# Kernel tuning notes

Measured on AMD Instinct MI355X. Metric: run time of the kernel, lower is better.

## Reference

```python
import jax, jax.numpy as jnp
import numpy as np
from jax.ops import segment_sum

N_NODES = 100000
N_EDGES = 1600000
N_GRAPHS = 128
HIDDEN = 128
N_CLASSES = 10


def setup_inputs() -> dict:
    key = jax.random.key(0)
    ks = jax.random.split(key, 8)
    src = jax.random.randint(ks[0], (N_EDGES,), 0, N_NODES, dtype=jnp.int32)
    dst = jax.random.randint(ks[1], (N_EDGES,), 0, N_NODES, dtype=jnp.int32)
    graph_ids = jnp.sort(jax.random.randint(ks[2], (N_NODES,), 0, N_GRAPHS, dtype=jnp.int32))
    W1 = jax.random.normal(ks[3], (1, HIDDEN), dtype=jnp.float32)
    b1 = jnp.zeros((HIDDEN,), jnp.float32)
    W2 = jax.random.normal(ks[4], (HIDDEN, HIDDEN), dtype=jnp.float32) * 0.05
    b2 = jnp.zeros((HIDDEN,), jnp.float32)
    Wc = jax.random.normal(ks[5], (HIDDEN, N_CLASSES), dtype=jnp.float32) * 0.05
    bc = jnp.zeros((N_CLASSES,), jnp.float32)
    return {"src": src, "dst": dst, "graph_ids": graph_ids,
            "W1": W1, "b1": b1, "W2": W2, "b2": b2, "Wc": Wc, "bc": bc}


def _graph_conv(h, src, dst, norm_src, norm_dst, W, b, n_nodes):
    # DGL GraphConv, norm='both': D_out^{-1/2} gather -> scatter-sum -> W -> D_in^{-1/2} -> +b
    hs = h * norm_src[:, None]
    agg = segment_sum(hs[src], dst, num_segments=n_nodes)  # [N, F_in]
    return agg @ W * norm_dst[:, None] + b


def reference(src, dst, graph_ids, W1, b1, W2, b2, Wc, bc):
    n_nodes = graph_ids.shape[0]
    ones_e = jnp.ones(src.shape[0], jnp.float32)
    indeg = segment_sum(ones_e, dst, num_segments=n_nodes)
    outdeg = segment_sum(ones_e, src, num_segments=n_nodes)
    norm_src = jnp.clip(outdeg, 1.0, None) ** -0.5
    norm_dst = jnp.clip(indeg, 1.0, None) ** -0.5

    h = indeg[:, None]  # node feature = in-degree, [N, 1]
    h = jax.nn.relu(_graph_conv(h, src, dst, norm_src, norm_dst, W1, b1, n_nodes))
    h = jax.nn.relu(_graph_conv(h, src, dst, norm_src, norm_dst, W2, b2, n_nodes))

    # dgl.mean_nodes: per-graph mean pooling
    sums = segment_sum(h, graph_ids, num_segments=N_GRAPHS)          # [G, H]
    cnts = segment_sum(jnp.ones(n_nodes, jnp.float32), graph_ids, num_segments=N_GRAPHS)
    hg = sums / jnp.clip(cnts, 1.0, None)[:, None]
    return hg @ Wc + bc  # [G, n_classes]
```

## Files before the change

kernel.cpp:

```cpp
#include <hip/hip_runtime.h>

#define N_NODES   100000
#define N_EDGES   1600000
#define N_GRAPHS  128
#define HIDDEN    128
#define N_CLASSES 10

#define BSH   9
#define BSZ   512
#define NBUCK 196
#define CAP   16384
#define PCH   4096

typedef unsigned int   uint;
typedef unsigned short ushort;
typedef unsigned char  uchar;
typedef unsigned long long ull;

__global__ __launch_bounds__(256)
void k_part(const int* __restrict__ src, const int* __restrict__ dst,
            unsigned* __restrict__ bcur1, unsigned* __restrict__ bcur2,
            unsigned* __restrict__ tmp1, ushort* __restrict__ tmp2, int nE) {
    __shared__ unsigned histD[256], histS[256], scanT[256];
    __shared__ unsigned lcurD[256], lcurS[256], baseD[256], baseS[256];
    __shared__ unsigned stag1[PCH];
    __shared__ ushort   stag2[PCH];
    __shared__ uchar    stagB1[PCH], stagB2[PCH];
    int t = threadIdx.x;
    int e0 = blockIdx.x * PCH;
    int e1 = min(e0 + PCH, nE);
    histD[t] = 0; histS[t] = 0;
    __syncthreads();
    for (int e = e0 + t; e < e1; e += 256) {
        atomicAdd(&histD[dst[e] >> BSH], 1u);
        atomicAdd(&histS[src[e] >> BSH], 1u);
    }
    __syncthreads();
    unsigned vD = histD[t];
    scanT[t] = vD; __syncthreads();
    for (int off = 1; off < 256; off <<= 1) {
        unsigned add = (t >= off) ? scanT[t - off] : 0u;
        __syncthreads();
        scanT[t] += add;
        __syncthreads();
    }
    unsigned exD = scanT[t] - vD;
    if (vD > 0) { unsigned g = atomicAdd(&bcur1[t], vD); baseD[t] = (unsigned)t * CAP + g - exD; }
    lcurD[t] = exD;
    __syncthreads();
    unsigned vS = histS[t];
    scanT[t] = vS; __syncthreads();
    for (int off = 1; off < 256; off <<= 1) {
        unsigned add = (t >= off) ? scanT[t - off] : 0u;
        __syncthreads();
        scanT[t] += add;
        __syncthreads();
    }
    unsigned exS = scanT[t] - vS;
    if (vS > 0) { unsigned g = atomicAdd(&bcur2[t], vS); baseS[t] = (unsigned)t * CAP + g - exS; }
    lcurS[t] = exS;
    __syncthreads();
    for (int e = e0 + t; e < e1; e += 256) {
        int d = dst[e], s = src[e];
        int bd = d >> BSH, bs = s >> BSH;
        unsigned p1 = atomicAdd(&lcurD[bd], 1u);
        stag1[p1]  = ((unsigned)(d & (BSZ - 1)) << 17) | (unsigned)s;
        stagB1[p1] = (uchar)bd;
        unsigned p2 = atomicAdd(&lcurS[bs], 1u);
        stag2[p2]  = (ushort)(s & (BSZ - 1));
        stagB2[p2] = (uchar)bs;
    }
    __syncthreads();
    int cntE = e1 - e0;
    for (int i = t; i < cntE; i += 256) {
        unsigned b = stagB1[i];
        unsigned a = baseD[b] + (unsigned)i;
        if (a < (b + 1u) * CAP) tmp1[a] = stag1[i];
    }
    for (int i = t; i < cntE; i += 256) {
        unsigned b = stagB2[i];
        unsigned a = baseS[b] + (unsigned)i;
        if (a < (b + 1u) * CAP) tmp2[a] = stag2[i];
    }
}

__global__ __launch_bounds__(1024)
void k_ind_hs0(const unsigned* __restrict__ bcur1, const unsigned* __restrict__ tmp1,
               const unsigned* __restrict__ bcur2, const ushort* __restrict__ tmp2,
               unsigned* __restrict__ indeg, float* __restrict__ ns,
               float* __restrict__ hs0) {
    __shared__ unsigned cin[BSZ], cout[BSZ];
    int b = blockIdx.x, t = threadIdx.x;
    if (t < BSZ) { cin[t] = 0; cout[t] = 0; }
    __syncthreads();
    unsigned f1 = min(bcur1[b], (unsigned)CAP);
    const unsigned* tp1 = tmp1 + (size_t)b * CAP;
    for (unsigned i = t; i < f1; i += 1024) atomicAdd(&cin[tp1[i] >> 17], 1u);
    unsigned f2 = min(bcur2[b], (unsigned)CAP);
    const ushort* tp2 = tmp2 + (size_t)b * CAP;
    for (unsigned i = t; i < f2; i += 1024) atomicAdd(&cout[tp2[i]], 1u);
    __syncthreads();
    if (t < BSZ) {
        int n = b * BSZ + t;
        if (n < N_NODES) {
            unsigned ci = cin[t], co = cout[t];
            float nsv = rsqrtf(fmaxf((float)co, 1.0f));
            indeg[n] = ci;
            ns[n]    = nsv;
            hs0[n]   = (float)ci * nsv;
        }
    }
}

__global__ void k_segtable(const float* __restrict__ W1, const float* __restrict__ b1,
                           const float* __restrict__ W2,
                           float* __restrict__ U, float* __restrict__ V,
                           float* __restrict__ ts) {
    __shared__ float s[128];
    int t = threadIdx.x;
    {
        float w = W1[t], bb = b1[t];
        s[t] = (w != 0.0f) ? (-bb / w) : 1e30f;
    }
    __syncthreads();
    for (int k = 2; k <= 128; k <<= 1) {
        for (int j = k >> 1; j > 0; j >>= 1) {
            int ixj = t ^ j;
            if (ixj > t) {
                float a = s[t], bb = s[ixj];
                bool up = ((t & k) == 0);
                if (up ? (a > bb) : (a < bb)) { s[t] = bb; s[ixj] = a; }
            }
            __syncthreads();
        }
    }
    if (blockIdx.x == 0) ts[t] = s[t];
    int sg = blockIdx.x;
    float a_rep;
    if (sg == 0)        a_rep = s[0]   - 1.0f;
    else if (sg == 128) a_rep = s[127] + 1.0f;
    else                a_rep = 0.5f * (s[sg - 1] + s[sg]);
    float u = 0.0f, v = 0.0f;
    for (int j = 0; j < 128; ++j) {
        float w = W1[j], bb = b1[j];
        if (a_rep * w + bb > 0.0f) {
            float w2 = W2[j * HIDDEN + t];
            u += w * w2;
            v += bb * w2;
        }
    }
    U[sg * HIDDEN + t] = u;
    V[sg * HIDDEN + t] = v;
}

__global__ __launch_bounds__(1024)
void k_conv1_info(const unsigned* __restrict__ bcur1, const unsigned* __restrict__ tmp1,
                  const float* __restrict__ hs0, const unsigned* __restrict__ indeg,
                  const float* __restrict__ ns, const float* __restrict__ ts,
                  float4* __restrict__ info) {
    __shared__ float acc[BSZ];
    __shared__ float sts[128];
    int b = blockIdx.x, t = threadIdx.x;
    if (t < BSZ) acc[t] = 0.0f;
    if (t < 128) sts[t] = ts[t];
    __syncthreads();
    unsigned f1 = min(bcur1[b], (unsigned)CAP);
    const unsigned* tp = tmp1 + (size_t)b * CAP;
    for (unsigned i = t; i < f1; i += 1024) {
        unsigned e = tp[i];
        atomicAdd(&acc[e >> 17], hs0[e & 0x1FFFFu]);
    }
    __syncthreads();
    if (t < BSZ) {
        int n = b * BSZ + t;
        if (n < N_NODES) {
            float nd = rsqrtf(fmaxf((float)indeg[n], 1.0f));
            float a  = acc[t] * nd;
            float nsv = ns[n];
            int sg = 0;
            #pragma unroll
            for (int j = 0; j < 128; ++j) sg += (sts[j] < a) ? 1 : 0;
            info[n] = make_float4(nsv * a, nsv, __int_as_float(sg), nd);
        }
    }
}

__global__ __launch_bounds__(1024)
void k_conv2_pool(const unsigned* __restrict__ bcur1, const unsigned* __restrict__ tmp1,
                  const float4* __restrict__ info, const unsigned* __restrict__ indeg,
                  const float* __restrict__ U, const float* __restrict__ V,
                  const int* __restrict__ graph_ids, const float* __restrict__ b2,
                  float* __restrict__ pool, float* __restrict__ cnt) {
    __shared__ float sc[BSZ], sn2[BSZ];
    __shared__ ull   ssq[BSZ];
    __shared__ float sND[BSZ];
    __shared__ int   sGr[BSZ];
    int b = blockIdx.x, t = threadIdx.x;
    if (t < BSZ) { sc[t] = 0.0f; sn2[t] = 0.0f; ssq[t] = 0ull; }
    __syncthreads();
    unsigned f1 = min(bcur1[b], (unsigned)CAP);
    const unsigned* tp = tmp1 + (size_t)b * CAP;
    for (unsigned i = t; i < f1; i += 1024) {
        unsigned e = tp[i];
        unsigned dl = e >> 17, s = e & 0x1FFFFu;
        float4 nf = info[s];
        unsigned sg = (unsigned)__float_as_int(nf.z);
        atomicAdd(&sc[dl],  nf.x);
        atomicAdd(&sn2[dl], nf.y);
        atomicAdd(&ssq[dl], ((ull)(sg * sg) << 32) | (ull)sg);
    }
    if (t < BSZ) {
        int n = b * BSZ + t;
        if (n < N_NODES) { sND[t] = info[n].w; sGr[t] = graph_ids[n]; }
    }
    __syncthreads();

    int w = t >> 6, lane = t & 63;
    int base = b * BSZ;
    float bb0 = b2[lane], bb1 = b2[64 + lane];
    int gcur = -1;
    float racc0 = 0.0f, racc1 = 0.0f, cl = 0.0f;

    for (int i = w * 32; i < w * 32 + 32; ++i) {
        int n = base + i;
        if (n >= N_NODES) break;
        unsigned cntN = indeg[n];
        ull pk = ssq[i];
        unsigned S1 = (unsigned)pk, S2 = (unsigned)(pk >> 32);
        float acc0, acc1;
        if ((ull)cntN * S2 == (ull)S1 * S1) {
            unsigned sg = cntN ? (S1 / cntN) : 0u;
            float A = sc[i], B = sn2[i];
            const float* Ur = U + sg * HIDDEN;
            const float* Vr = V + sg * HIDDEN;
            acc0 = A * Ur[lane]      + B * Vr[lane];
            acc1 = A * Ur[64 + lane] + B * Vr[64 + lane];
        } else {
            acc0 = 0.0f; acc1 = 0.0f;
            for (unsigned j = 0; j < f1; ++j) {
                unsigned e = tp[j];
                if ((int)(e >> 17) == i) {
                    float4 nf = info[e & 0x1FFFFu];
                    unsigned sg = (unsigned)__float_as_int(nf.z);
                    const float* Ur = U + sg * HIDDEN;
                    const float* Vr = V + sg * HIDDEN;
                    acc0 += nf.x * Ur[lane]      + nf.y * Vr[lane];
                    acc1 += nf.x * Ur[64 + lane] + nf.y * Vr[64 + lane];
                }
            }
        }
        float nd = sND[i];
        float r0 = fmaxf(nd * acc0 + bb0, 0.0f);
        float r1 = fmaxf(nd * acc1 + bb1, 0.0f);
        int g = sGr[i];
        if (g != gcur) {
            if (gcur >= 0) {
                atomicAdd(&pool[gcur * HIDDEN + lane],      racc0);
                atomicAdd(&pool[gcur * HIDDEN + 64 + lane], racc1);
                if (lane == 0) atomicAdd(&cnt[gcur], cl);
            }
            gcur = g; racc0 = 0.0f; racc1 = 0.0f; cl = 0.0f;
        }
        racc0 += r0; racc1 += r1; cl += 1.0f;
    }
    if (gcur >= 0) {
        atomicAdd(&pool[gcur * HIDDEN + lane],      racc0);
        atomicAdd(&pool[gcur * HIDDEN + 64 + lane], racc1);
        if (lane == 0) atomicAdd(&cnt[gcur], cl);
    }
}

__global__ void k_final(const float* __restrict__ pool, const float* __restrict__ cnt,
                        const float* __restrict__ Wc, const float* __restrict__ bc,
                        float* __restrict__ out) {
    int t = blockIdx.x * blockDim.x + threadIdx.x;
    if (t >= N_GRAPHS * N_CLASSES) return;
    int g = t / N_CLASSES, c = t % N_CLASSES;
    float inv = 1.0f / fmaxf(cnt[g], 1.0f);
    float acc = bc[c];
    for (int j = 0; j < HIDDEN; ++j)
        acc += pool[g * HIDDEN + j] * inv * Wc[j * N_CLASSES + c];
    out[t] = acc;
}

extern "C" void kernel_launch(void* const* d_in, const int* in_sizes, int n_in,
                              void* d_out, int out_size, void* d_ws, size_t ws_size,
                              hipStream_t stream) {
    const int*   src       = (const int*)d_in[0];
    const int*   dst       = (const int*)d_in[1];
    const int*   graph_ids = (const int*)d_in[2];
    const float* W1        = (const float*)d_in[3];
    const float* b1        = (const float*)d_in[4];
    const float* W2        = (const float*)d_in[5];
    const float* b2        = (const float*)d_in[6];
    const float* Wc        = (const float*)d_in[7];
    const float* bc        = (const float*)d_in[8];
    float* out = (float*)d_out;

    char* ws = (char*)d_ws;
    size_t off = 0;
    auto alloc = [&](size_t elems) { void* p = ws + off; off += elems * 4; return p; };

    unsigned* bcur1 = (unsigned*)alloc(256);
    unsigned* bcur2 = (unsigned*)alloc(256);
    float*    pool  = (float*)   alloc(N_GRAPHS * HIDDEN);
    float*    cnt   = (float*)   alloc(N_GRAPHS);
    size_t zero_bytes = off;
    float4*   info  = (float4*)  alloc((size_t)N_NODES * 4);
    unsigned* tmp1  = (unsigned*)alloc((size_t)NBUCK * CAP);
    ushort*   tmp2  = (ushort*)  alloc((size_t)NBUCK * CAP / 2);
    unsigned* indeg = (unsigned*)alloc(N_NODES);
    float*    nsA   = (float*)   alloc(N_NODES);
    float*    hs0   = (float*)   alloc(N_NODES);
    float*    ts    = (float*)   alloc(128);
    float*    U     = (float*)   alloc(129 * HIDDEN);
    float*    V     = (float*)   alloc(129 * HIDDEN);

    hipMemsetAsync(d_ws, 0, zero_bytes, stream);

    int pblocks = (N_EDGES + PCH - 1) / PCH;
    k_part      <<<pblocks, 256, 0, stream>>>(src, dst, bcur1, bcur2, tmp1, tmp2, N_EDGES);
    k_ind_hs0   <<<NBUCK, 1024, 0, stream>>>(bcur1, tmp1, bcur2, tmp2, indeg, nsA, hs0);
    k_segtable  <<<129, 128, 0, stream>>>(W1, b1, W2, U, V, ts);
    k_conv1_info<<<NBUCK, 1024, 0, stream>>>(bcur1, tmp1, hs0, indeg, nsA, ts, info);
    k_conv2_pool<<<NBUCK, 1024, 0, stream>>>(bcur1, tmp1, info, indeg, U, V, graph_ids, b2, pool, cnt);
    k_final     <<<(N_GRAPHS * N_CLASSES + 255) / 256, 256, 0, stream>>>(pool, cnt, Wc, bc, out);
}
```

Before: 201.3 us.

## Build per-bucket CSR and switch conv kernels to per-node gather

The in-degree kernel now prefix-scans per-node in-degrees within each bucket and scatters source ids into a CSR layout. Both conv kernels then run one thread per node, summing over that node's CSR row instead of doing shared-memory atomics over the bucket's edge list. Conv2 replaces the sum/sum-of-squares uniformity test with a min/max segment check. This also lets the fallback path walk only the node's own edges rather than rescanning the whole bucket. The cost is an extra CSR write pass plus per-thread loops whose length varies with degree.

After: 191.2 us. 5.0% less time.

```diff
diff --git a/kernel.cpp b/kernel.cpp
--- a/kernel.cpp
+++ b/kernel.cpp
@@ -15,7 +15,6 @@
 typedef unsigned int   uint;
 typedef unsigned short ushort;
 typedef unsigned char  uchar;
-typedef unsigned long long ull;
 
 __global__ __launch_bounds__(256)
 void k_part(const int* __restrict__ src, const int* __restrict__ dst,
@@ -85,11 +84,12 @@
 }
 
 __global__ __launch_bounds__(1024)
-void k_ind_hs0(const unsigned* __restrict__ bcur1, const unsigned* __restrict__ tmp1,
+void k_ind_csr(const unsigned* __restrict__ bcur1, const unsigned* __restrict__ tmp1,
                const unsigned* __restrict__ bcur2, const ushort* __restrict__ tmp2,
                unsigned* __restrict__ indeg, float* __restrict__ ns,
-               float* __restrict__ hs0) {
-    __shared__ unsigned cin[BSZ], cout[BSZ];
+               float* __restrict__ hs0, int* __restrict__ rs,
+               int* __restrict__ csr) {
+    __shared__ unsigned cin[BSZ], cout[BSZ], pref[BSZ], lcur[BSZ];
     int b = blockIdx.x, t = threadIdx.x;
     if (t < BSZ) { cin[t] = 0; cout[t] = 0; }
     __syncthreads();
@@ -100,7 +100,18 @@
     const ushort* tp2 = tmp2 + (size_t)b * CAP;
     for (unsigned i = t; i < f2; i += 1024) atomicAdd(&cout[tp2[i]], 1u);
     __syncthreads();
+    unsigned v = (t < BSZ) ? cin[t] : 0u;
+    if (t < BSZ) pref[t] = v;
+    __syncthreads();
+    for (int off = 1; off < BSZ; off <<= 1) {
+        unsigned add = (t < BSZ && t >= off) ? pref[t - off] : 0u;
+        __syncthreads();
+        if (t < BSZ) pref[t] += add;
+        __syncthreads();
+    }
     if (t < BSZ) {
+        unsigned excl = pref[t] - v;
+        lcur[t] = excl;
         int n = b * BSZ + t;
         if (n < N_NODES) {
             unsigned ci = cin[t], co = cout[t];
@@ -108,7 +119,15 @@
             indeg[n] = ci;
             ns[n]    = nsv;
             hs0[n]   = (float)ci * nsv;
-        }
+            rs[n]    = (int)(b * CAP + excl);
+        }
+    }
+    __syncthreads();
+    int* cb = csr + (size_t)b * CAP;
+    for (unsigned i = t; i < f1; i += 1024) {
+        unsigned e = tp1[i];
+        unsigned pos = atomicAdd(&lcur[e >> 17], 1u);
+        cb[pos] = (int)(e & 0x1FFFFu);
     }
 }
 
@@ -153,105 +172,96 @@
     V[sg * HIDDEN + t] = v;
 }
 
-__global__ __launch_bounds__(1024)
-void k_conv1_info(const unsigned* __restrict__ bcur1, const unsigned* __restrict__ tmp1,
+__global__ __launch_bounds__(256)
+void k_conv1_info(const int* __restrict__ rs, const int* __restrict__ csr,
                   const float* __restrict__ hs0, const unsigned* __restrict__ indeg,
                   const float* __restrict__ ns, const float* __restrict__ ts,
-                  float4* __restrict__ info) {
-    __shared__ float acc[BSZ];
+                  float4* __restrict__ info, int nN) {
     __shared__ float sts[128];
-    int b = blockIdx.x, t = threadIdx.x;
-    if (t < BSZ) acc[t] = 0.0f;
-    if (t < 128) sts[t] = ts[t];
-    __syncthreads();
-    unsigned f1 = min(bcur1[b], (unsigned)CAP);
-    const unsigned* tp = tmp1 + (size_t)b * CAP;
-    for (unsigned i = t; i < f1; i += 1024) {
-        unsigned e = tp[i];
-        atomicAdd(&acc[e >> 17], hs0[e & 0x1FFFFu]);
-    }
-    __syncthreads();
-    if (t < BSZ) {
-        int n = b * BSZ + t;
-        if (n < N_NODES) {
-            float nd = rsqrtf(fmaxf((float)indeg[n], 1.0f));
-            float a  = acc[t] * nd;
-            float nsv = ns[n];
-            int sg = 0;
-            #pragma unroll
-            for (int j = 0; j < 128; ++j) sg += (sts[j] < a) ? 1 : 0;
-            info[n] = make_float4(nsv * a, nsv, __int_as_float(sg), nd);
-        }
-    }
-}
-
-__global__ __launch_bounds__(1024)
-void k_conv2_pool(const unsigned* __restrict__ bcur1, const unsigned* __restrict__ tmp1,
+    if (threadIdx.x < 128) sts[threadIdx.x] = ts[threadIdx.x];
+    __syncthreads();
+    int n = blockIdx.x * 256 + threadIdx.x;
+    if (n >= nN) return;
+    int r0 = rs[n];
+    int c  = (int)indeg[n];
+    float a = 0.0f;
+    #pragma unroll 4
+    for (int k = 0; k < c; ++k) a += hs0[csr[r0 + k]];
+    float nd = rsqrtf(fmaxf((float)c, 1.0f));
+    a *= nd;
+    float nsv = ns[n];
+    int sg = 0;
+    #pragma unroll
+    for (int j = 0; j < 128; ++j) sg += (sts[j] < a) ? 1 : 0;
+    info[n] = make_float4(nsv * a, nsv, __int_as_float(sg), nd);
+}
+
+__global__ __launch_bounds__(256)
+void k_conv2_pool(const int* __restrict__ rs, const int* __restrict__ csr,
                   const float4* __restrict__ info, const unsigned* __restrict__ indeg,
                   const float* __restrict__ U, const float* __restrict__ V,
                   const int* __restrict__ graph_ids, const float* __restrict__ b2,
-                  float* __restrict__ pool, float* __restrict__ cnt) {
-    __shared__ float sc[BSZ], sn2[BSZ];
-    __shared__ ull   ssq[BSZ];
-    __shared__ float sND[BSZ];
-    __shared__ int   sGr[BSZ];
-    int b = blockIdx.x, t = threadIdx.x;
-    if (t < BSZ) { sc[t] = 0.0f; sn2[t] = 0.0f; ssq[t] = 0ull; }
-    __syncthreads();
-    unsigned f1 = min(bcur1[b], (unsigned)CAP);
-    const unsigned* tp = tmp1 + (size_t)b * CAP;
-    for (unsigned i = t; i < f1; i += 1024) {
-        unsigned e = tp[i];
-        unsigned dl = e >> 17, s = e & 0x1FFFFu;
-        float4 nf = info[s];
-        unsigned sg = (unsigned)__float_as_int(nf.z);
-        atomicAdd(&sc[dl],  nf.x);
-        atomicAdd(&sn2[dl], nf.y);
-        atomicAdd(&ssq[dl], ((ull)(sg * sg) << 32) | (ull)sg);
-    }
-    if (t < BSZ) {
-        int n = b * BSZ + t;
-        if (n < N_NODES) { sND[t] = info[n].w; sGr[t] = graph_ids[n]; }
+                  float* __restrict__ pool, float* __restrict__ cnt, int nN) {
+    __shared__ float sA[256], sB[256], sND[256];
+    __shared__ int   sSg[256], sGr[256], sR[256], sC[256];
+    int blockBase = blockIdx.x * 256;
+    int t = threadIdx.x;
+    int n = blockBase + t;
+
+    if (n < nN) {
+        int r0 = rs[n], c = (int)indeg[n];
+        float A = 0.0f, B = 0.0f;
+        int mn = 255, mx = 0;
+        #pragma unroll 4
+        for (int k = 0; k < c; ++k) {
+            float4 nf = info[csr[r0 + k]];
+            int sg = __float_as_int(nf.z);
+            A += nf.x; B += nf.y;
+            mn = min(mn, sg); mx = max(mx, sg);
+        }
+        sA[t] = A; sB[t] = B;
+        sSg[t] = (mn << 8) | mx;
+        sR[t] = r0; sC[t] = c;
+        sND[t] = info[n].w;
+        sGr[t] = graph_ids[n];
     }
     __syncthreads();
 
     int w = t >> 6, lane = t & 63;
-    int base = b * BSZ;
+    int n0 = blockBase + 64 * w;
+    if (n0 >= nN) return;
+    int n1 = min(n0 + 64, nN);
+
     float bb0 = b2[lane], bb1 = b2[64 + lane];
     int gcur = -1;
     float racc0 = 0.0f, racc1 = 0.0f, cl = 0.0f;
 
-    for (int i = w * 32; i < w * 32 + 32; ++i) {
-        int n = base + i;
-        if (n >= N_NODES) break;
-        unsigned cntN = indeg[n];
-        ull pk = ssq[i];
-        unsigned S1 = (unsigned)pk, S2 = (unsigned)(pk >> 32);
+    for (int node = n0; node < n1; ++node) {
+        int i = node - blockBase;
+        int pk = sSg[i], mn = pk >> 8, mx = pk & 255;
         float acc0, acc1;
-        if ((ull)cntN * S2 == (ull)S1 * S1) {
-            unsigned sg = cntN ? (S1 / cntN) : 0u;
-            float A = sc[i], B = sn2[i];
+        if (mn >= mx) {
+            int sg = min(mn, 128);
+            float A = sA[i], B = sB[i];
             const float* Ur = U + sg * HIDDEN;
             const float* Vr = V + sg * HIDDEN;
             acc0 = A * Ur[lane]      + B * Vr[lane];
             acc1 = A * Ur[64 + lane] + B * Vr[64 + lane];
         } else {
             acc0 = 0.0f; acc1 = 0.0f;
-            for (unsigned j = 0; j < f1; ++j) {
-                unsigned e = tp[j];
-                if ((int)(e >> 17) == i) {
-                    float4 nf = info[e & 0x1FFFFu];
-                    unsigned sg = (unsigned)__float_as_int(nf.z);
-                    const float* Ur = U + sg * HIDDEN;
-                    const float* Vr = V + sg * HIDDEN;
-                    acc0 += nf.x * Ur[lane]      + nf.y * Vr[lane];
-                    acc1 += nf.x * Ur[64 + lane] + nf.y * Vr[64 + lane];
-                }
+            int r0 = sR[i], c = sC[i];
+            for (int k = 0; k < c; ++k) {
+                float4 nf = info[csr[r0 + k]];
+                int sg = __float_as_int(nf.z);
+                const float* Ur = U + sg * HIDDEN;
+                const float* Vr = V + sg * HIDDEN;
+                acc0 += nf.x * Ur[lane]      + nf.y * Vr[lane];
+                acc1 += nf.x * Ur[64 + lane] + nf.y * Vr[64 + lane];
             }
         }
         float nd = sND[i];
-        float r0 = fmaxf(nd * acc0 + bb0, 0.0f);
-        float r1 = fmaxf(nd * acc1 + bb1, 0.0f);
+        float r0v = fmaxf(nd * acc0 + bb0, 0.0f);
+        float r1v = fmaxf(nd * acc1 + bb1, 0.0f);
         int g = sGr[i];
         if (g != gcur) {
             if (gcur >= 0) {
@@ -261,7 +271,7 @@
             }
             gcur = g; racc0 = 0.0f; racc1 = 0.0f; cl = 0.0f;
         }
-        racc0 += r0; racc1 += r1; cl += 1.0f;
+        racc0 += r0v; racc1 += r1v; cl += 1.0f;
     }
     if (gcur >= 0) {
         atomicAdd(&pool[gcur * HIDDEN + lane],      racc0);
@@ -309,6 +319,8 @@
     float4*   info  = (float4*)  alloc((size_t)N_NODES * 4);
     unsigned* tmp1  = (unsigned*)alloc((size_t)NBUCK * CAP);
     ushort*   tmp2  = (ushort*)  alloc((size_t)NBUCK * CAP / 2);
+    int*      csr   = (int*)     alloc((size_t)NBUCK * CAP);
+    int*      rs    = (int*)     alloc(N_NODES);
     unsigned* indeg = (unsigned*)alloc(N_NODES);
     float*    nsA   = (float*)   alloc(N_NODES);
     float*    hs0   = (float*)   alloc(N_NODES);
@@ -319,10 +331,11 @@
     hipMemsetAsync(d_ws, 0, zero_bytes, stream);
 
     int pblocks = (N_EDGES + PCH - 1) / PCH;
+    int nblocks = (N_NODES + 255) / 256;
     k_part      <<<pblocks, 256, 0, stream>>>(src, dst, bcur1, bcur2, tmp1, tmp2, N_EDGES);
-    k_ind_hs0   <<<NBUCK, 1024, 0, stream>>>(bcur1, tmp1, bcur2, tmp2, indeg, nsA, hs0);
+    k_ind_csr   <<<NBUCK, 1024, 0, stream>>>(bcur1, tmp1, bcur2, tmp2, indeg, nsA, hs0, rs, csr);
     k_segtable  <<<129, 128, 0, stream>>>(W1, b1, W2, U, V, ts);
-    k_conv1_info<<<NBUCK, 1024, 0, stream>>>(bcur1, tmp1, hs0, indeg, nsA, ts, info);
-    k_conv2_pool<<<NBUCK, 1024, 0, stream>>>(bcur1, tmp1, info, indeg, U, V, graph_ids, b2, pool, cnt);
+    k_conv1_info<<<nblocks, 256, 0, stream>>>(rs, csr, hs0, indeg, nsA, ts, info, N_NODES);
+    k_conv2_pool<<<nblocks, 256, 0, stream>>>(rs, csr, info, indeg, U, V, graph_ids, b2, pool, cnt, N_NODES);
     k_final     <<<(N_GRAPHS * N_CLASSES + 255) / 256, 256, 0, stream>>>(pool, cnt, Wc, bc, out);
 }
```
